# Kernel tuning notes

Measured on AMD Instinct MI355X. Metric: run time of the kernel, lower is better.

## Reference

```python
import jax, jax.numpy as jnp
import numpy as np

B = 262144
MA = [128, 128]
MB = [128, 128]


def krone_linear(x_a, x_b, wa, wb, ba, bb):
    # slice inputs to each branch's in_features (torch slices the wider branch)
    ia, ib = wa.shape[1], wb.shape[1]
    x_a = x_a[:, :ia]
    x_b = x_b[:, :ib]
    h_a = x_a @ wa.T + ba
    h_b = x_b @ wb.T + bb
    # zero-pad the narrower output so both branches share a width (static shapes)
    oa, ob = wa.shape[0], wb.shape[0]
    if oa > ob:
        h_b = jnp.pad(h_b, ((0, 0), (0, oa - ob)))
    elif ob > oa:
        h_a = jnp.pad(h_a, ((0, 0), (0, ob - oa)))
    return h_a, h_b


def krone_softmax(x_a, x_b, fa, fb):
    x_a = x_a[:, :fa]
    x_b = x_b[:, :fb]
    # vectorized per-row Kronecker product: kron(a, b)[i*fb + j] = a[i]*b[j]
    y = (x_a[:, :, None] * x_b[:, None, :]).reshape(x_a.shape[0], fa * fb)
    return jax.nn.softmax(y, axis=1)


def setup_inputs() -> dict:
    key = jax.random.key(0)
    ks = jax.random.split(key, 13)
    s = 0.1
    inp = {
        "x": jax.random.normal(ks[0], (2, B, 2), dtype=jnp.float32),
        "w1a": jax.random.normal(ks[1], (MA[0], 2), dtype=jnp.float32) * s,
        "w1b": jax.random.normal(ks[2], (MB[0], 2), dtype=jnp.float32) * s,
        "b1a": jax.random.normal(ks[3], (MA[0],), dtype=jnp.float32) * s,
        "b1b": jax.random.normal(ks[4], (MB[0],), dtype=jnp.float32) * s,
        "w2a": jax.random.normal(ks[5], (MA[1], MA[0]), dtype=jnp.float32) * s,
        "w2b": jax.random.normal(ks[6], (MB[1], MB[0]), dtype=jnp.float32) * s,
        "b2a": jax.random.normal(ks[7], (MA[1],), dtype=jnp.float32) * s,
        "b2b": jax.random.normal(ks[8], (MB[1],), dtype=jnp.float32) * s,
        "w3a": jax.random.normal(ks[9], (1, MA[1]), dtype=jnp.float32) * s,
        "w3b": jax.random.normal(ks[10], (3, MB[1]), dtype=jnp.float32) * s,
        "b3a": jax.random.normal(ks[11], (1,), dtype=jnp.float32) * s,
        "b3b": jax.random.normal(ks[12], (3,), dtype=jnp.float32) * s,
    }
    return inp


def reference(x, w1a, w1b, b1a, b1b, w2a, w2b, b2a, b2b, w3a, w3b, b3a, b3b):
    x_a, x_b = x[0], x[1]
    h_a, h_b = krone_linear(x_a, x_b, w1a, w1b, b1a, b1b)
    h_a, h_b = jax.nn.relu(h_a), jax.nn.relu(h_b)
    h_a, h_b = krone_linear(h_a, h_b, w2a, w2b, b2a, b2b)
    h_a, h_b = jax.nn.relu(h_a), jax.nn.relu(h_b)
    h_a, h_b = krone_linear(h_a, h_b, w3a, w3b, b3a, b3b)
    return krone_softmax(h_a, h_b, 1, 3)
```

## Files before the change

kernel.cpp:

```cpp
#include <hip/hip_runtime.h>
#include <hip/hip_bf16.h>


#define BTOT 262144
#define NBLK (BTOT / 512)

typedef __attribute__((ext_vector_type(4))) float floatx4;
typedef __attribute__((ext_vector_type(8))) short bf16x8;
typedef __attribute__((ext_vector_type(4))) int  intx4;

#define OFF_W2   0
#define OFF_W1A  32768
#define OFF_W1B  35072
#define OFF_B2A  37376
#define OFF_B2B  37888
#define OFF_W3A  38400
#define OFF_W3B  38912
#define OFF_SA   40960
#define LDS_TOTAL 43008

static __device__ __forceinline__ int pack2bf(float lo, float hi) {
    int r;
    asm("v_cvt_pk_bf16_f32 %0, %1, %2" : "=v"(r) : "v"(lo), "v"(hi));
    return r;
}

#define SEL4(a0, a1, a2, a3, i) \
    ((i) == 0 ? (a0) : (i) == 1 ? (a1) : (i) == 2 ? (a2) : (a3))

template <int CTRL>
static __device__ __forceinline__ float dppadd(float v) {
    int t = __builtin_amdgcn_update_dpp(0, __builtin_bit_cast(int, v),
                                        CTRL, 0xF, 0xF, true);
    return v + __builtin_bit_cast(float, t);
}
static __device__ __forceinline__ float redcol(float v) {
    v = dppadd<0xB1>(v);
    v = dppadd<0x4E>(v);
    v = dppadd<0x141>(v);
    v = dppadd<0x140>(v);
    return v;
}

static __device__ __forceinline__ int w1slot(int k) { return k + (k >> 3); }

static __device__ __forceinline__ void pack_w2(
        unsigned char* smem, int tid, const float* __restrict__ w2) {
    const float4* w2p = (const float4*)w2;
    #pragma unroll
    for (int i = 0; i < 8; ++i) {
        int n  = (tid & 15) | (i << 4);
        int k4 = tid >> 4;
        float4 f = w2p[n * 32 + k4];
        int k = k4 * 4;
        int s = k >> 5;
        int j0 = k & 7;
        int l = ((k & 31) >> 3) * 16 + (n & 15);
        int2 pkd;
        pkd.x = pack2bf(f.x, f.y);
        pkd.y = pack2bf(f.z, f.w);
        *(int2*)(smem + OFF_W2 + (s * 8 + (n >> 4)) * 1024 + l * 16 + j0 * 2) = pkd;
    }
}

static __device__ __forceinline__ void stage_small(
        unsigned char* smem, int tid, int offW1, int offB2,
        const float* __restrict__ w1, const float* __restrict__ b1,
        const float* __restrict__ b2) {
    if (tid < 128) {
        ((float4*)(smem + offW1))[w1slot(tid)] =
            make_float4(w1[2 * tid], w1[2 * tid + 1], b1[tid], 0.f);
        ((float*)(smem + offB2))[tid] = b2[tid];
    }
}

#define GEMM_CHUNK(acc, XV, W1p, W2p, B2p)                                     \
    {                                                                          \
        _Pragma("unroll")                                                      \
        for (int t = 0; t < 8; ++t) {                                          \
            float b2n = (B2p)[t * 16 + col];                                   \
            floatx4 bi = (floatx4){b2n, b2n, b2n, b2n};                        \
            _Pragma("unroll")                                                  \
            for (int mt = 0; mt < 2; ++mt) acc[t][mt] = bi;                    \
        }                                                                      \
        _Pragma("unroll")                                                      \
        for (int s = 0; s < 4; ++s) {                                          \
            intx4 af[2];                                                       \
            const int bslot = s * 36 + quad * 9;                               \
            _Pragma("unroll")                                                  \
            for (int j2 = 0; j2 < 4; ++j2) {                                   \
                float4 c0 = (W1p)[bslot + 2 * j2];                             \
                float4 c1 = (W1p)[bslot + 2 * j2 + 1];                         \
                _Pragma("unroll")                                              \
                for (int mt = 0; mt < 2; ++mt) {                               \
                    float h0 = fmaxf(fmaf((XV)[mt].x, c0.x,                    \
                                fmaf((XV)[mt].y, c0.y, c0.z)), 0.f);           \
                    float h1 = fmaxf(fmaf((XV)[mt].x, c1.x,                    \
                                fmaf((XV)[mt].y, c1.y, c1.z)), 0.f);           \
                    af[mt][j2] = pack2bf(h0, h1);                              \
                }                                                              \
            }                                                                  \
            _Pragma("unroll")                                                  \
            for (int t = 0; t < 8; ++t) {                                      \
                bf16x8 bfr = (W2p)[(s * 8 + t) * 64 + lane];                   \
                _Pragma("unroll")                                              \
                for (int mt = 0; mt < 2; ++mt)                                 \
                    acc[t][mt] = __builtin_amdgcn_mfma_f32_16x16x32_bf16(      \
                        __builtin_bit_cast(bf16x8, af[mt]), bfr,               \
                        acc[t][mt], 0, 0, 0);                                  \
            }                                                                  \
        }                                                                      \
    }

__global__ __launch_bounds__(512, 4)
void krone_fused(const float* __restrict__ x,
                 const float* __restrict__ w1a, const float* __restrict__ w1b,
                 const float* __restrict__ b1a, const float* __restrict__ b1b,
                 const float* __restrict__ w2a, const float* __restrict__ w2b,
                 const float* __restrict__ b2a, const float* __restrict__ b2b,
                 const float* __restrict__ w3a, const float* __restrict__ w3b,
                 const float* __restrict__ b3a, const float* __restrict__ b3b,
                 float* __restrict__ out) {
    __shared__ __align__(16) unsigned char smem[LDS_TOTAL];

    const int tid  = threadIdx.x;
    const int lane = tid & 63;
    const int wave = tid >> 6;
    const int quad = lane >> 4;
    const int col  = lane & 15;
    const int wbase = blockIdx.x * 512 + wave * 64;

    const bf16x8* W2  = (const bf16x8*)(smem + OFF_W2);
    const float4* W1A = (const float4*)(smem + OFF_W1A);
    const float4* W1B = (const float4*)(smem + OFF_W1B);
    const float*  B2A = (const float*)(smem + OFF_B2A);
    const float*  B2B = (const float*)(smem + OFF_B2B);
    const float*  W3A = (const float*)(smem + OFF_W3A);
    const float4* W3T = (const float4*)(smem + OFF_W3B);
    float*        SA  = (float*)(smem + OFF_SA);
    const float2* xA = (const float2*)x;
    const float2* xB = xA + BTOT;

    const float b3a_ = b3a[0];
    const float b30 = b3b[0], b31 = b3b[1], b32 = b3b[2];

    float2 xv[4];
    #pragma unroll
    for (int c = 0; c < 2; ++c)
        #pragma unroll
        for (int mt = 0; mt < 2; ++mt)
            xv[c * 2 + mt] = xA[wbase + c * 32 + mt * 16 + col];

    pack_w2(smem, tid, w2a);
    stage_small(smem, tid, OFF_W1A, OFF_B2A, w1a, b1a, b2a);
    stage_small(smem, tid, OFF_W1B, OFF_B2B, w1b, b1b, b2b);
    if (tid < 128) ((float*)(smem + OFF_W3A))[tid] = w3a[tid];
    if (tid < 384) {
        int j = tid >> 7, n = tid & 127;
        ((float*)(smem + OFF_W3B))[n * 4 + j] = w3b[tid];
    }
    __syncthreads();

    #pragma unroll
    for (int c = 0; c < 2; ++c) {
        __builtin_amdgcn_sched_barrier(0);
        floatx4 acc[8][2];
        GEMM_CHUNK(acc, xv + 2 * c, W1A, W2, B2A);
        __builtin_amdgcn_sched_barrier(0);

        float pa[2][4] = {};
        #pragma unroll
        for (int t = 0; t < 8; ++t) {
            float w3n = W3A[t * 16 + col];
            #pragma unroll
            for (int mt = 0; mt < 2; ++mt)
                #pragma unroll
                for (int r = 0; r < 4; ++r)
                    pa[mt][r] = fmaf(w3n, fmaxf(acc[t][mt][r], 0.f), pa[mt][r]);
        }
        #pragma unroll
        for (int mt = 0; mt < 2; ++mt)
            #pragma unroll
            for (int r = 0; r < 4; ++r) pa[mt][r] = redcol(pa[mt][r]);
        __builtin_amdgcn_sched_barrier(0);

        if (col < 4) {
            #pragma unroll
            for (int mt = 0; mt < 2; ++mt) {
                int sl = mt * 16 + quad * 4 + col;
                SA[wave * 64 + c * 32 + sl] =
                    SEL4(pa[mt][0], pa[mt][1], pa[mt][2], pa[mt][3], col) + b3a_;
            }
        }
        __builtin_amdgcn_sched_barrier(0);
    }

    #pragma unroll
    for (int c = 0; c < 2; ++c)
        #pragma unroll
        for (int mt = 0; mt < 2; ++mt)
            xv[c * 2 + mt] = xB[wbase + c * 32 + mt * 16 + col];

    __syncthreads();
    pack_w2(smem, tid, w2b);
    __syncthreads();

    #pragma unroll
    for (int c = 0; c < 2; ++c) {
        __builtin_amdgcn_sched_barrier(0);
        floatx4 acc[8][2];
        GEMM_CHUNK(acc, xv + 2 * c, W1B, W2, B2B);
        __builtin_amdgcn_sched_barrier(0);

        #pragma unroll
        for (int mt = 0; mt < 2; ++mt) {
            float p0[4] = {}, p1[4] = {}, p2[4] = {};
            #pragma unroll
            for (int t = 0; t < 8; ++t) {
                float4 w3v = W3T[t * 16 + col];
                #pragma unroll
                for (int r = 0; r < 4; ++r) {
                    float h = fmaxf(acc[t][mt][r], 0.f);
                    p0[r] = fmaf(w3v.x, h, p0[r]);
                    p1[r] = fmaf(w3v.y, h, p1[r]);
                    p2[r] = fmaf(w3v.z, h, p2[r]);
                }
            }
            #pragma unroll
            for (int r = 0; r < 4; ++r) {
                p0[r] = redcol(p0[r]);
                p1[r] = redcol(p1[r]);
                p2[r] = redcol(p2[r]);
            }
            if (col < 4) {
                int sl = mt * 16 + quad * 4 + col;
                float t0 = SEL4(p0[0], p0[1], p0[2], p0[3], col) + b30;
                float t1 = SEL4(p1[0], p1[1], p1[2], p1[3], col) + b31;
                float t2 = SEL4(p2[0], p2[1], p2[2], p2[3], col) + b32;
                float sa = SA[wave * 64 + c * 32 + sl];
                float y0 = sa * t0, y1 = sa * t1, y2 = sa * t2;
                float m = fmaxf(y0, fmaxf(y1, y2));
                float e0 = __expf(y0 - m), e1 = __expf(y1 - m), e2 = __expf(y2 - m);
                float rs = 1.f / (e0 + e1 + e2);
                long o = (long)(wbase + c * 32 + sl) * 3;
                out[o]     = e0 * rs;
                out[o + 1] = e1 * rs;
                out[o + 2] = e2 * rs;
            }
        }
        __builtin_amdgcn_sched_barrier(0);
    }
}

extern "C" void kernel_launch(void* const* d_in, const int* in_sizes, int n_in,
                              void* d_out, int out_size, void* d_ws, size_t ws_size,
                              hipStream_t stream) {
    const float* x   = (const float*)d_in[0];
    const float* w1a = (const float*)d_in[1];
    const float* w1b = (const float*)d_in[2];
    const float* b1a = (const float*)d_in[3];
    const float* b1b = (const float*)d_in[4];
    const float* w2a = (const float*)d_in[5];
    const float* w2b = (const float*)d_in[6];
    const float* b2a = (const float*)d_in[7];
    const float* b2b = (const float*)d_in[8];
    const float* w3a = (const float*)d_in[9];
    const float* w3b = (const float*)d_in[10];
    const float* b3a = (const float*)d_in[11];
    const float* b3b = (const float*)d_in[12];
    float* out = (float*)d_out;

    krone_fused<<<NBLK, 512, 0, stream>>>(x, w1a, w1b, b1a, b1b, w2a, w2b,
                                          b2a, b2b, w3a, w3b, b3a, b3b, out);
}
```

Measured before the change: 105.7 us.

## Stage both W2 matrices upfront, fold bias into MFMA, transpose-reduce epilogue

Packs both branch W2 matrices into LDS at kernel start, which removes the mid-kernel repack and its two block barriers. LDS use grows from about 43KB to 77KB, which may reduce occupancy. The layer-2 bias is now fed as the first MFMA accumulator, and layer 1 uses packed two-wide FMAs on a reorganized W1 layout. The column reductions use a transposing DPP reduce (red4) so each lane ends with a distinct row sum, and the softmax uses exp2 with a prescaled log2e, a fast reciprocal, and spreads the output stores across 12 lanes.

```diff
diff --git a/kernel.cpp b/kernel.cpp
--- a/kernel.cpp
+++ b/kernel.cpp
@@ -6,27 +6,28 @@
 #define NBLK (BTOT / 512)
 
 typedef __attribute__((ext_vector_type(4))) float floatx4;
+typedef __attribute__((ext_vector_type(2))) float floatx2;
 typedef __attribute__((ext_vector_type(8))) short bf16x8;
 typedef __attribute__((ext_vector_type(4))) int  intx4;
 
-#define OFF_W2   0
-#define OFF_W1A  32768
-#define OFF_W1B  35072
-#define OFF_B2A  37376
-#define OFF_B2B  37888
-#define OFF_W3A  38400
-#define OFF_W3B  38912
-#define OFF_SA   40960
-#define LDS_TOTAL 43008
+#define OFF_W2A  0
+#define OFF_W2B  32768
+#define OFF_PA   65536
+#define OFF_PB   66560
+#define OFF_ZA   67584
+#define OFF_ZB   68096
+#define OFF_B2A  68608
+#define OFF_B2B  70656
+#define OFF_W3A  72704
+#define OFF_W3T  73216
+#define OFF_SA   75264
+#define LDS_TOTAL 77312
 
 static __device__ __forceinline__ int pack2bf(float lo, float hi) {
     int r;
     asm("v_cvt_pk_bf16_f32 %0, %1, %2" : "=v"(r) : "v"(lo), "v"(hi));
     return r;
 }
-
-#define SEL4(a0, a1, a2, a3, i) \
-    ((i) == 0 ? (a0) : (i) == 1 ? (a1) : (i) == 2 ? (a2) : (a3))
 
 template <int CTRL>
 static __device__ __forceinline__ float dppadd(float v) {
@@ -34,18 +35,22 @@
                                         CTRL, 0xF, 0xF, true);
     return v + __builtin_bit_cast(float, t);
 }
-static __device__ __forceinline__ float redcol(float v) {
-    v = dppadd<0xB1>(v);
-    v = dppadd<0x4E>(v);
-    v = dppadd<0x141>(v);
-    v = dppadd<0x140>(v);
-    return v;
-}
-
-static __device__ __forceinline__ int w1slot(int k) { return k + (k >> 3); }
+
+static __device__ __forceinline__ float red4(float a0, float a1, float a2,
+                                             float a3, int col) {
+    float s0 = dppadd<0xB1>(a0), s1 = dppadd<0xB1>(a1);
+    float s2 = dppadd<0xB1>(a2), s3 = dppadd<0xB1>(a3);
+    float u0 = (col & 1) ? s1 : s0;
+    float u1 = (col & 1) ? s3 : s2;
+    float v0 = dppadd<0x4E>(u0), v1 = dppadd<0x4E>(u1);
+    float w  = (col & 2) ? v1 : v0;
+    w = dppadd<0x124>(w);
+    w = dppadd<0x128>(w);
+    return w;
+}
 
 static __device__ __forceinline__ void pack_w2(
-        unsigned char* smem, int tid, const float* __restrict__ w2) {
+        unsigned char* dst, int tid, const float* __restrict__ w2) {
     const float4* w2p = (const float4*)w2;
     #pragma unroll
     for (int i = 0; i < 8; ++i) {
@@ -59,55 +64,60 @@
         int2 pkd;
         pkd.x = pack2bf(f.x, f.y);
         pkd.y = pack2bf(f.z, f.w);
-        *(int2*)(smem + OFF_W2 + (s * 8 + (n >> 4)) * 1024 + l * 16 + j0 * 2) = pkd;
-    }
-}
-
-static __device__ __forceinline__ void stage_small(
-        unsigned char* smem, int tid, int offW1, int offB2,
-        const float* __restrict__ w1, const float* __restrict__ b1,
-        const float* __restrict__ b2) {
-    if (tid < 128) {
-        ((float4*)(smem + offW1))[w1slot(tid)] =
-            make_float4(w1[2 * tid], w1[2 * tid + 1], b1[tid], 0.f);
-        ((float*)(smem + offB2))[tid] = b2[tid];
-    }
-}
-
-#define GEMM_CHUNK(acc, XV, W1p, W2p, B2p)                                     \
+        *(int2*)(dst + (s * 8 + (n >> 4)) * 1024 + l * 16 + j0 * 2) = pkd;
+    }
+}
+
+static __device__ __forceinline__ void stage_w1(
+        unsigned char* smem, int offP, int offZ, int e,
+        const float* __restrict__ w1, const float* __restrict__ b1) {
+    floatx4 g = ((const floatx4*)w1)[e];
+    ((floatx4*)(smem + offP))[e] = (floatx4){g.x, g.z, g.y, g.w};
+    ((floatx2*)(smem + offZ))[e] = (floatx2){b1[2 * e], b1[2 * e + 1]};
+}
+
+#define GEMM_CHUNK(acc, XV, Pp, Zp, W2p, B2Rp)                                 \
     {                                                                          \
+        floatx2 xx[2], xy[2];                                                  \
         _Pragma("unroll")                                                      \
-        for (int t = 0; t < 8; ++t) {                                          \
-            float b2n = (B2p)[t * 16 + col];                                   \
-            floatx4 bi = (floatx4){b2n, b2n, b2n, b2n};                        \
-            _Pragma("unroll")                                                  \
-            for (int mt = 0; mt < 2; ++mt) acc[t][mt] = bi;                    \
+        for (int mt = 0; mt < 2; ++mt) {                                       \
+            xx[mt] = (floatx2){(XV)[mt].x, (XV)[mt].x};                        \
+            xy[mt] = (floatx2){(XV)[mt].y, (XV)[mt].y};                        \
         }                                                                      \
         _Pragma("unroll")                                                      \
         for (int s = 0; s < 4; ++s) {                                          \
             intx4 af[2];                                                       \
-            const int bslot = s * 36 + quad * 9;                               \
+            const int ebase = s * 16 + quad * 4;                               \
             _Pragma("unroll")                                                  \
             for (int j2 = 0; j2 < 4; ++j2) {                                   \
-                float4 c0 = (W1p)[bslot + 2 * j2];                             \
-                float4 c1 = (W1p)[bslot + 2 * j2 + 1];                         \
+                floatx4 P = (Pp)[ebase + j2];                                  \
+                floatx2 Z = (Zp)[ebase + j2];                                  \
                 _Pragma("unroll")                                              \
                 for (int mt = 0; mt < 2; ++mt) {                               \
-                    float h0 = fmaxf(fmaf((XV)[mt].x, c0.x,                    \
-                                fmaf((XV)[mt].y, c0.y, c0.z)), 0.f);           \
-                    float h1 = fmaxf(fmaf((XV)[mt].x, c1.x,                    \
-                                fmaf((XV)[mt].y, c1.y, c1.z)), 0.f);           \
-                    af[mt][j2] = pack2bf(h0, h1);                              \
+                    floatx2 tt = __builtin_elementwise_fma(                    \
+                        xy[mt], (floatx2){P.z, P.w}, Z);                       \
+                    floatx2 h = __builtin_elementwise_fma(                     \
+                        xx[mt], (floatx2){P.x, P.y}, tt);                      \
+                    af[mt][j2] = pack2bf(fmaxf(h.x, 0.f), fmaxf(h.y, 0.f));    \
                 }                                                              \
             }                                                                  \
             _Pragma("unroll")                                                  \
             for (int t = 0; t < 8; ++t) {                                      \
                 bf16x8 bfr = (W2p)[(s * 8 + t) * 64 + lane];                   \
-                _Pragma("unroll")                                              \
-                for (int mt = 0; mt < 2; ++mt)                                 \
-                    acc[t][mt] = __builtin_amdgcn_mfma_f32_16x16x32_bf16(      \
-                        __builtin_bit_cast(bf16x8, af[mt]), bfr,               \
-                        acc[t][mt], 0, 0, 0);                                  \
+                if (s == 0) {                                                  \
+                    floatx4 bias = (B2Rp)[t * 16 + col];                       \
+                    _Pragma("unroll")                                          \
+                    for (int mt = 0; mt < 2; ++mt)                             \
+                        acc[t][mt] = __builtin_amdgcn_mfma_f32_16x16x32_bf16(  \
+                            __builtin_bit_cast(bf16x8, af[mt]), bfr,           \
+                            bias, 0, 0, 0);                                    \
+                } else {                                                       \
+                    _Pragma("unroll")                                          \
+                    for (int mt = 0; mt < 2; ++mt)                             \
+                        acc[t][mt] = __builtin_amdgcn_mfma_f32_16x16x32_bf16(  \
+                            __builtin_bit_cast(bf16x8, af[mt]), bfr,           \
+                            acc[t][mt], 0, 0, 0);                              \
+                }                                                              \
             }                                                                  \
         }                                                                      \
     }
@@ -130,14 +140,17 @@
     const int col  = lane & 15;
     const int wbase = blockIdx.x * 512 + wave * 64;
 
-    const bf16x8* W2  = (const bf16x8*)(smem + OFF_W2);
-    const float4* W1A = (const float4*)(smem + OFF_W1A);
-    const float4* W1B = (const float4*)(smem + OFF_W1B);
-    const float*  B2A = (const float*)(smem + OFF_B2A);
-    const float*  B2B = (const float*)(smem + OFF_B2B);
-    const float*  W3A = (const float*)(smem + OFF_W3A);
-    const float4* W3T = (const float4*)(smem + OFF_W3B);
-    float*        SA  = (float*)(smem + OFF_SA);
+    const bf16x8*  W2A = (const bf16x8*)(smem + OFF_W2A);
+    const bf16x8*  W2B = (const bf16x8*)(smem + OFF_W2B);
+    const floatx4* PA  = (const floatx4*)(smem + OFF_PA);
+    const floatx4* PB  = (const floatx4*)(smem + OFF_PB);
+    const floatx2* ZA  = (const floatx2*)(smem + OFF_ZA);
+    const floatx2* ZB  = (const floatx2*)(smem + OFF_ZB);
+    const floatx4* B2RA = (const floatx4*)(smem + OFF_B2A);
+    const floatx4* B2RB = (const floatx4*)(smem + OFF_B2B);
+    const float*   W3A = (const float*)(smem + OFF_W3A);
+    const floatx4* W3T = (const floatx4*)(smem + OFF_W3T);
+    float*         SA  = (float*)(smem + OFF_SA);
     const float2* xA = (const float2*)x;
     const float2* xB = xA + BTOT;
 
@@ -151,13 +164,25 @@
         for (int mt = 0; mt < 2; ++mt)
             xv[c * 2 + mt] = xA[wbase + c * 32 + mt * 16 + col];
 
-    pack_w2(smem, tid, w2a);
-    stage_small(smem, tid, OFF_W1A, OFF_B2A, w1a, b1a, b2a);
-    stage_small(smem, tid, OFF_W1B, OFF_B2B, w1b, b1b, b2b);
-    if (tid < 128) ((float*)(smem + OFF_W3A))[tid] = w3a[tid];
+    pack_w2(smem + OFF_W2A, tid, w2a);
+    pack_w2(smem + OFF_W2B, tid, w2b);
+    if (tid < 64) {
+        stage_w1(smem, OFF_PA, OFF_ZA, tid, w1a, b1a);
+    } else if (tid < 128) {
+        stage_w1(smem, OFF_PB, OFF_ZB, tid - 64, w1b, b1b);
+    } else if (tid < 256) {
+        int e = tid - 128; float b = b2a[e];
+        ((floatx4*)(smem + OFF_B2A))[e] = (floatx4){b, b, b, b};
+    } else if (tid < 384) {
+        int e = tid - 256; float b = b2b[e];
+        ((floatx4*)(smem + OFF_B2B))[e] = (floatx4){b, b, b, b};
+    } else {
+        int e = tid - 384;
+        ((float*)(smem + OFF_W3A))[e] = w3a[e];
+    }
     if (tid < 384) {
         int j = tid >> 7, n = tid & 127;
-        ((float*)(smem + OFF_W3B))[n * 4 + j] = w3b[tid];
+        ((float*)(smem + OFF_W3T))[n * 4 + j] = w3b[tid];
     }
     __syncthreads();
 
@@ -165,7 +190,7 @@
     for (int c = 0; c < 2; ++c) {
         __builtin_amdgcn_sched_barrier(0);
         floatx4 acc[8][2];
-        GEMM_CHUNK(acc, xv + 2 * c, W1A, W2, B2A);
+        GEMM_CHUNK(acc, xv + 2 * c, PA, ZA, W2A, B2RA);
         __builtin_amdgcn_sched_barrier(0);
 
         float pa[2][4] = {};
@@ -179,17 +204,11 @@
                     pa[mt][r] = fmaf(w3n, fmaxf(acc[t][mt][r], 0.f), pa[mt][r]);
         }
         #pragma unroll
-        for (int mt = 0; mt < 2; ++mt)
-            #pragma unroll
-            for (int r = 0; r < 4; ++r) pa[mt][r] = redcol(pa[mt][r]);
-        __builtin_amdgcn_sched_barrier(0);
-
-        if (col < 4) {
-            #pragma unroll
-            for (int mt = 0; mt < 2; ++mt) {
+        for (int mt = 0; mt < 2; ++mt) {
+            float w = red4(pa[mt][0], pa[mt][1], pa[mt][2], pa[mt][3], col);
+            if (col < 4) {
                 int sl = mt * 16 + quad * 4 + col;
-                SA[wave * 64 + c * 32 + sl] =
-                    SEL4(pa[mt][0], pa[mt][1], pa[mt][2], pa[mt][3], col) + b3a_;
+                SA[wave * 64 + c * 32 + sl] = (w + b3a_) * 1.44269504089f;
             }
         }
         __builtin_amdgcn_sched_barrier(0);
@@ -201,15 +220,11 @@
         for (int mt = 0; mt < 2; ++mt)
             xv[c * 2 + mt] = xB[wbase + c * 32 + mt * 16 + col];
 
-    __syncthreads();
-    pack_w2(smem, tid, w2b);
-    __syncthreads();
-
     #pragma unroll
     for (int c = 0; c < 2; ++c) {
         __builtin_amdgcn_sched_barrier(0);
         floatx4 acc[8][2];
-        GEMM_CHUNK(acc, xv + 2 * c, W1B, W2, B2B);
+        GEMM_CHUNK(acc, xv + 2 * c, PB, ZB, W2B, B2RB);
         __builtin_amdgcn_sched_barrier(0);
 
         #pragma unroll
@@ -217,7 +232,7 @@
             float p0[4] = {}, p1[4] = {}, p2[4] = {};
             #pragma unroll
             for (int t = 0; t < 8; ++t) {
-                float4 w3v = W3T[t * 16 + col];
+                floatx4 w3v = W3T[t * 16 + col];
                 #pragma unroll
                 for (int r = 0; r < 4; ++r) {
                     float h = fmaxf(acc[t][mt][r], 0.f);
@@ -226,26 +241,19 @@
                     p2[r] = fmaf(w3v.z, h, p2[r]);
                 }
             }
-            #pragma unroll
-            for (int r = 0; r < 4; ++r) {
-                p0[r] = redcol(p0[r]);
-                p1[r] = redcol(p1[r]);
-                p2[r] = redcol(p2[r]);
-            }
-            if (col < 4) {
-                int sl = mt * 16 + quad * 4 + col;
-                float t0 = SEL4(p0[0], p0[1], p0[2], p0[3], col) + b30;
-                float t1 = SEL4(p1[0], p1[1], p1[2], p1[3], col) + b31;
-                float t2 = SEL4(p2[0], p2[1], p2[2], p2[3], col) + b32;
-                float sa = SA[wave * 64 + c * 32 + sl];
-                float y0 = sa * t0, y1 = sa * t1, y2 = sa * t2;
-                float m = fmaxf(y0, fmaxf(y1, y2));
-                float e0 = __expf(y0 - m), e1 = __expf(y1 - m), e2 = __expf(y2 - m);
-                float rs = 1.f / (e0 + e1 + e2);
-                long o = (long)(wbase + c * 32 + sl) * 3;
-                out[o]     = e0 * rs;
-                out[o + 1] = e1 * rs;
-                out[o + 2] = e2 * rs;
+            float t0 = red4(p0[0], p0[1], p0[2], p0[3], col) + b30;
+            float t1 = red4(p1[0], p1[1], p1[2], p1[3], col) + b31;
+            float t2 = red4(p2[0], p2[1], p2[2], p2[3], col) + b32;
+            int sl = mt * 16 + quad * 4 + (col & 3);
+            float sa = SA[wave * 64 + c * 32 + sl];
+            float y0 = sa * t0, y1 = sa * t1, y2 = sa * t2;
+            float m = fmaxf(y0, fmaxf(y1, y2));
+            float e0 = exp2f(y0 - m), e1 = exp2f(y1 - m), e2 = exp2f(y2 - m);
+            float rs = __builtin_amdgcn_rcpf(e0 + e1 + e2);
+            float ev = (col >= 8) ? e2 : ((col >= 4) ? e1 : e0);
+            if (col < 12) {
+                long o = (long)(wbase + c * 32 + sl) * 3 + (col >> 2);
+                out[o] = ev * rs;
             }
         }
         __builtin_amdgcn_sched_barrier(0);
```

Measured after the change: 120.8 us. 14.3% more time.

## Stage both W2 matrices upfront, merge DPP reductions, and spread softmax stores across lanes

Applied to the files above, without the earlier changes.

Packs both branch W2 weight matrices into LDS at kernel start. This removes the two block-wide barriers and the mid-kernel restaging of W2 between the A and B branches. The per-column DPP reductions are merged into a red4 routine that reduces four row values together, with selects between steps, so fewer DPP ops are issued. The softmax uses exp2 with log2(e) folded into the stored A-branch scalar, and a hardware reciprocal. Output stores are split across 12 lanes (one component each) instead of 4 lanes writing 3 values. LDS use grows from about 43KB to about 76KB per block, which may cut occupancy below the 4 blocks per CU requested in launch bounds.

```diff
diff --git a/kernel.cpp b/kernel.cpp
--- a/kernel.cpp
+++ b/kernel.cpp
@@ -9,24 +9,22 @@
 typedef __attribute__((ext_vector_type(8))) short bf16x8;
 typedef __attribute__((ext_vector_type(4))) int  intx4;
 
-#define OFF_W2   0
-#define OFF_W1A  32768
-#define OFF_W1B  35072
-#define OFF_B2A  37376
-#define OFF_B2B  37888
-#define OFF_W3A  38400
-#define OFF_W3B  38912
-#define OFF_SA   40960
-#define LDS_TOTAL 43008
+#define OFF_W2A  0
+#define OFF_W2B  32768
+#define OFF_W1A  65536
+#define OFF_W1B  67840
+#define OFF_B2A  70144
+#define OFF_B2B  70656
+#define OFF_W3A  71168
+#define OFF_W3T  71680
+#define OFF_SA   73728
+#define LDS_TOTAL 75776
 
 static __device__ __forceinline__ int pack2bf(float lo, float hi) {
     int r;
     asm("v_cvt_pk_bf16_f32 %0, %1, %2" : "=v"(r) : "v"(lo), "v"(hi));
     return r;
 }
-
-#define SEL4(a0, a1, a2, a3, i) \
-    ((i) == 0 ? (a0) : (i) == 1 ? (a1) : (i) == 2 ? (a2) : (a3))
 
 template <int CTRL>
 static __device__ __forceinline__ float dppadd(float v) {
@@ -34,18 +32,24 @@
                                         CTRL, 0xF, 0xF, true);
     return v + __builtin_bit_cast(float, t);
 }
-static __device__ __forceinline__ float redcol(float v) {
-    v = dppadd<0xB1>(v);
-    v = dppadd<0x4E>(v);
-    v = dppadd<0x141>(v);
-    v = dppadd<0x140>(v);
-    return v;
+
+static __device__ __forceinline__ float red4(float a0, float a1, float a2,
+                                             float a3, int col) {
+    float s0 = dppadd<0xB1>(a0), s1 = dppadd<0xB1>(a1);
+    float s2 = dppadd<0xB1>(a2), s3 = dppadd<0xB1>(a3);
+    float u0 = (col & 1) ? s1 : s0;
+    float u1 = (col & 1) ? s3 : s2;
+    float v0 = dppadd<0x4E>(u0), v1 = dppadd<0x4E>(u1);
+    float w  = (col & 2) ? v1 : v0;
+    w = dppadd<0x124>(w);
+    w = dppadd<0x128>(w);
+    return w;
 }
 
 static __device__ __forceinline__ int w1slot(int k) { return k + (k >> 3); }
 
 static __device__ __forceinline__ void pack_w2(
-        unsigned char* smem, int tid, const float* __restrict__ w2) {
+        unsigned char* dst, int tid, const float* __restrict__ w2) {
     const float4* w2p = (const float4*)w2;
     #pragma unroll
     for (int i = 0; i < 8; ++i) {
@@ -59,7 +63,7 @@
         int2 pkd;
         pkd.x = pack2bf(f.x, f.y);
         pkd.y = pack2bf(f.z, f.w);
-        *(int2*)(smem + OFF_W2 + (s * 8 + (n >> 4)) * 1024 + l * 16 + j0 * 2) = pkd;
+        *(int2*)(dst + (s * 8 + (n >> 4)) * 1024 + l * 16 + j0 * 2) = pkd;
     }
 }
 
@@ -130,13 +134,14 @@
     const int col  = lane & 15;
     const int wbase = blockIdx.x * 512 + wave * 64;
 
-    const bf16x8* W2  = (const bf16x8*)(smem + OFF_W2);
+    const bf16x8* W2A = (const bf16x8*)(smem + OFF_W2A);
+    const bf16x8* W2B = (const bf16x8*)(smem + OFF_W2B);
     const float4* W1A = (const float4*)(smem + OFF_W1A);
     const float4* W1B = (const float4*)(smem + OFF_W1B);
     const float*  B2A = (const float*)(smem + OFF_B2A);
     const float*  B2B = (const float*)(smem + OFF_B2B);
     const float*  W3A = (const float*)(smem + OFF_W3A);
-    const float4* W3T = (const float4*)(smem + OFF_W3B);
+    const floatx4* W3T = (const floatx4*)(smem + OFF_W3T);
     float*        SA  = (float*)(smem + OFF_SA);
     const float2* xA = (const float2*)x;
     const float2* xB = xA + BTOT;
@@ -151,13 +156,14 @@
         for (int mt = 0; mt < 2; ++mt)
             xv[c * 2 + mt] = xA[wbase + c * 32 + mt * 16 + col];
 
-    pack_w2(smem, tid, w2a);
+    pack_w2(smem + OFF_W2A, tid, w2a);
+    pack_w2(smem + OFF_W2B, tid, w2b);
     stage_small(smem, tid, OFF_W1A, OFF_B2A, w1a, b1a, b2a);
     stage_small(smem, tid, OFF_W1B, OFF_B2B, w1b, b1b, b2b);
     if (tid < 128) ((float*)(smem + OFF_W3A))[tid] = w3a[tid];
     if (tid < 384) {
         int j = tid >> 7, n = tid & 127;
-        ((float*)(smem + OFF_W3B))[n * 4 + j] = w3b[tid];
+        ((float*)(smem + OFF_W3T))[n * 4 + j] = w3b[tid];
     }
     __syncthreads();
 
@@ -165,7 +171,7 @@
     for (int c = 0; c < 2; ++c) {
         __builtin_amdgcn_sched_barrier(0);
         floatx4 acc[8][2];
-        GEMM_CHUNK(acc, xv + 2 * c, W1A, W2, B2A);
+        GEMM_CHUNK(acc, xv + 2 * c, W1A, W2A, B2A);
         __builtin_amdgcn_sched_barrier(0);
 
         float pa[2][4] = {};
@@ -179,17 +185,11 @@
                     pa[mt][r] = fmaf(w3n, fmaxf(acc[t][mt][r], 0.f), pa[mt][r]);
         }
         #pragma unroll
-        for (int mt = 0; mt < 2; ++mt)
-            #pragma unroll
-            for (int r = 0; r < 4; ++r) pa[mt][r] = redcol(pa[mt][r]);
-        __builtin_amdgcn_sched_barrier(0);
-
-        if (col < 4) {
-            #pragma unroll
-            for (int mt = 0; mt < 2; ++mt) {
+        for (int mt = 0; mt < 2; ++mt) {
+            float w = red4(pa[mt][0], pa[mt][1], pa[mt][2], pa[mt][3], col);
+            if (col < 4) {
                 int sl = mt * 16 + quad * 4 + col;
-                SA[wave * 64 + c * 32 + sl] =
-                    SEL4(pa[mt][0], pa[mt][1], pa[mt][2], pa[mt][3], col) + b3a_;
+                SA[wave * 64 + c * 32 + sl] = (w + b3a_) * 1.44269504089f;
             }
         }
         __builtin_amdgcn_sched_barrier(0);
@@ -201,15 +201,11 @@
         for (int mt = 0; mt < 2; ++mt)
             xv[c * 2 + mt] = xB[wbase + c * 32 + mt * 16 + col];
 
-    __syncthreads();
-    pack_w2(smem, tid, w2b);
-    __syncthreads();
-
     #pragma unroll
     for (int c = 0; c < 2; ++c) {
         __builtin_amdgcn_sched_barrier(0);
         floatx4 acc[8][2];
-        GEMM_CHUNK(acc, xv + 2 * c, W1B, W2, B2B);
+        GEMM_CHUNK(acc, xv + 2 * c, W1B, W2B, B2B);
         __builtin_amdgcn_sched_barrier(0);
 
         #pragma unroll
@@ -217,7 +213,7 @@
             float p0[4] = {}, p1[4] = {}, p2[4] = {};
             #pragma unroll
             for (int t = 0; t < 8; ++t) {
-                float4 w3v = W3T[t * 16 + col];
+                floatx4 w3v = W3T[t * 16 + col];
                 #pragma unroll
                 for (int r = 0; r < 4; ++r) {
                     float h = fmaxf(acc[t][mt][r], 0.f);
@@ -226,26 +222,19 @@
                     p2[r] = fmaf(w3v.z, h, p2[r]);
                 }
             }
-            #pragma unroll
-            for (int r = 0; r < 4; ++r) {
-                p0[r] = redcol(p0[r]);
-                p1[r] = redcol(p1[r]);
-                p2[r] = redcol(p2[r]);
-            }
-            if (col < 4) {
-                int sl = mt * 16 + quad * 4 + col;
-                float t0 = SEL4(p0[0], p0[1], p0[2], p0[3], col) + b30;
-                float t1 = SEL4(p1[0], p1[1], p1[2], p1[3], col) + b31;
-                float t2 = SEL4(p2[0], p2[1], p2[2], p2[3], col) + b32;
-                float sa = SA[wave * 64 + c * 32 + sl];
-                float y0 = sa * t0, y1 = sa * t1, y2 = sa * t2;
-                float m = fmaxf(y0, fmaxf(y1, y2));
-                float e0 = __expf(y0 - m), e1 = __expf(y1 - m), e2 = __expf(y2 - m);
-                float rs = 1.f / (e0 + e1 + e2);
-                long o = (long)(wbase + c * 32 + sl) * 3;
-                out[o]     = e0 * rs;
-                out[o + 1] = e1 * rs;
-                out[o + 2] = e2 * rs;
+            float t0 = red4(p0[0], p0[1], p0[2], p0[3], col) + b30;
+            float t1 = red4(p1[0], p1[1], p1[2], p1[3], col) + b31;
+            float t2 = red4(p2[0], p2[1], p2[2], p2[3], col) + b32;
+            int sl = mt * 16 + quad * 4 + (col & 3);
+            float sa = SA[wave * 64 + c * 32 + sl];
+            float y0 = sa * t0, y1 = sa * t1, y2 = sa * t2;
+            float m = fmaxf(y0, fmaxf(y1, y2));
+            float e0 = exp2f(y0 - m), e1 = exp2f(y1 - m), e2 = exp2f(y2 - m);
+            float rs = __builtin_amdgcn_rcpf(e0 + e1 + e2);
+            float ev = (col >= 8) ? e2 : ((col >= 4) ? e1 : e0);
+            if (col < 12) {
+                long o = (long)(wbase + c * 32 + sl) * 3 + (col >> 2);
+                out[o] = ev * rs;
             }
         }
         __builtin_amdgcn_sched_barrier(0);
```

After: 108.5 us. +2.7%, slower.
